# Kernel tuning notes

Measured on AMD Instinct MI355X. Metric: run time of the kernel, lower is better.

## Reference

```python
import jax, jax.numpy as jnp
import numpy as np

EPS = 1e-12  # matches torch F.normalize eps
TEMPERATURE = 1.0


def _l2_normalize(x):
    n = jnp.sqrt(jnp.sum(x * x, axis=-1, keepdims=True))
    return x / jnp.maximum(n, EPS)


def setup_inputs() -> dict:
    key = jax.random.key(0)
    k1, k2 = jax.random.split(key)
    B, L, D, V = 2, 2048, 1024, 32000
    embeddings = jax.random.normal(k1, (B, L, D), dtype=jnp.float32)
    vocab_embeddings = jax.random.normal(k2, (V, D), dtype=jnp.float32)
    return {"embeddings": embeddings, "vocab_embeddings": vocab_embeddings, "k": 8}


def reference(embeddings, vocab_embeddings, k):
    """Soft KNN routing: cosine similarity -> top-k -> temperature softmax
    scattered into a full (B, L, V) probability distribution, plus hard
    argmax token ids (forward())."""
    B, L, D = embeddings.shape
    V = vocab_embeddings.shape[0]
    q = _l2_normalize(embeddings.reshape(-1, D))          # (N, D)
    vocab = _l2_normalize(vocab_embeddings)               # (V, D)
    sims = q @ vocab.T                                    # (N, V) cosine similarities
    topk_sim, topk_idx = jax.lax.top_k(sims, k)           # (N, k)
    probs_k = jax.nn.softmax(topk_sim / TEMPERATURE, axis=-1)
    N = q.shape[0]
    probs = jnp.zeros((N, V), dtype=probs_k.dtype)
    probs = probs.at[jnp.arange(N)[:, None], topk_idx].set(probs_k)
    probs = probs.reshape(B, L, V)                        # forward_soft output
    token_ids = topk_idx[:, 0].reshape(B, L)              # forward() hard routing (k=1)
    return probs, token_ids
```

## Files before the change

kernel.cpp:

```cpp
#include <hip/hip_runtime.h>
#include <math.h>

typedef unsigned short u16;
typedef unsigned int u32;
typedef unsigned char u8;
typedef long i64;
typedef float f32x16 __attribute__((ext_vector_type(16)));

static constexpr int N = 4096;
static constexpr int D = 1024;
static constexpr int V = 32000;
static constexpr int K = 8;
static constexpr int BM = 128;
static constexpr int BV = 256;
static constexpr int BK = 128;
static constexpr int NTILES = V / BV;
static constexpr int NG = 16;
static constexpr int NCAND = NG * K;
static constexpr int T24 = 24;
static constexpr int CPL = NCAND / 64;
static constexpr int GRID = (N / BM) * NG;
static constexpr u32 PSENT = 0x00800000u;

static constexpr size_t OUT_PROB_BYTES = (size_t)N * V * 4;
static constexpr size_t CAND_OFS = 83886080;
static constexpr size_t ZOFS = CAND_OFS + (size_t)N * NCAND * 4;
static constexpr size_t NZ4 = (OUT_PROB_BYTES - ZOFS) / 16;

static_assert(N % BM == 0 && V % BV == 0, "tiling");
static_assert(ZOFS % 16 == 0, "align");
static_assert(NZ4 == (size_t)209 * GRID * 256, "zero quota exact");

__device__ __forceinline__ u8 f2fp8(float f) {
  u32 u = __float_as_uint(f);
  u32 sign = (u >> 24) & 0x80u;
  u32 au = u & 0x7FFFFFFFu;
  if (au < 0x3D800000u) {
    int m = (int)(__uint_as_float(au) * 512.0f + 0.5f);
    return (u8)(sign | (u32)m);
  }
  au += 0x7FFFFu + ((au >> 20) & 1u);
  if (au >= 0x43E00000u) return (u8)(sign | 0x7Eu);
  u32 e = (au >> 23) - 120u;
  return (u8)(sign | (e << 3) | ((au >> 20) & 7u));
}
__device__ __forceinline__ u32 flipbits(float v) {
  u32 u = __float_as_uint(v);
  return u ^ (((u32)((int)u >> 31)) | 0x80000000u);
}
__device__ __forceinline__ float unpackval(u32 p) {
  u32 s = p | 2047u;
  u32 u = (s & 0x80000000u) ? (s ^ 0x80000000u) : ~s;
  return __uint_as_float(u);
}
__device__ __forceinline__ void insert8(u32 pv[K], u32 x) {
  if (x <= pv[K - 1]) return;
  bool g[K];
#pragma unroll
  for (int j = 0; j < K; ++j) g[j] = x > pv[j];
#pragma unroll
  for (int j = K - 1; j >= 1; --j)
    pv[j] = g[j - 1] ? pv[j - 1] : (g[j] ? x : pv[j]);
  if (g[0]) pv[0] = x;
}

__global__ void zero_kernel(float4* __restrict__ p, int n4) {
  int i = blockIdx.x * blockDim.x + threadIdx.x;
  int stride = gridDim.x * blockDim.x;
  float4 z = make_float4(0.f, 0.f, 0.f, 0.f);
  for (; i < n4; i += stride) p[i] = z;
}

__global__ void normcvt_kernel(const float* __restrict__ x, float* __restrict__ inv,
                               u32* __restrict__ o) {
  int row = blockIdx.x;
  const float4* xr = reinterpret_cast<const float4*>(x + (size_t)row * D);
  float4 v = xr[threadIdx.x];
  float ss = v.x * v.x + v.y * v.y + v.z * v.z + v.w * v.w;
#pragma unroll
  for (int off = 32; off > 0; off >>= 1) ss += __shfl_down(ss, off, 64);
  __shared__ float wsum[4];
  if ((threadIdx.x & 63) == 0) wsum[threadIdx.x >> 6] = ss;
  __syncthreads();
  __shared__ float s_inv;
  if (threadIdx.x == 0) {
    float t = wsum[0] + wsum[1] + wsum[2] + wsum[3];
    float iv = 1.0f / fmaxf(sqrtf(t), 1e-12f);
    inv[row] = iv;
    s_inv = iv;
  }
  __syncthreads();
  float s = s_inv * 16.0f;
  u32 b0 = f2fp8(v.x * s), b1 = f2fp8(v.y * s), b2 = f2fp8(v.z * s), b3 = f2fp8(v.w * s);
  o[row * (D / 4) + threadIdx.x] = b0 | (b1 << 8) | (b2 << 16) | (b3 << 24);
}

__global__ __launch_bounds__(256, 2)
void simtopk_kernel(const u8* __restrict__ qn, const u8* __restrict__ vn,
                    u32* __restrict__ cand, float4* __restrict__ zout) {
  __shared__ __align__(16) u8 sh[(BV + BM) * BK];

  u8* v_sh = sh;
  u8* q_sh = sh + BV * BK;

  const int tid = threadIdx.x;
  const int bid = blockIdx.x;
  const int u_ = bid >> 3;
  const int rb = u_ & 31;
  const int grp = (bid & 7) * 2 + (u_ >> 5);
  const int t0 = (grp * NTILES) >> 4;
  const int t1 = ((grp + 1) * NTILES) >> 4;
  const int rbase = rb * BM;
  const int wid = tid >> 6, l = tid & 63;
  const int wv = wid >> 1, wq = wid & 1;
  const int h = l >> 5, lid = l & 31;
  const int srow = l >> 3;
  const int sk = ((l & 7) ^ srow) << 4;

  const float4 zf4 = make_float4(0.f, 0.f, 0.f, 0.f);

  u32 pv[2][K];
#pragma unroll
  for (int n = 0; n < 2; ++n)
#pragma unroll
    for (int j = 0; j < K; ++j) pv[n][j] = PSENT;
  float tminf[2] = {-3.0e38f, -3.0e38f};

  for (int ti = t0; ti < t1; ++ti) {
    const int cb = (ti - t0) * BV;
    f32x16 acc[4][2];
#pragma unroll
    for (int m = 0; m < 4; ++m)
#pragma unroll
      for (int n = 0; n < 2; ++n)
#pragma unroll
        for (int r = 0; r < 16; ++r) acc[m][n][r] = 0.f;

    for (int kk = 0; kk < D / BK; ++kk) {
      __syncthreads();
      {
        int it = (ti - t0) * 8 + kk;
#pragma unroll
        for (int j = 0; j < 4; ++j) {
          int s = it * 4 + j;
          if (s < 209) zout[(size_t)s * (GRID * 256) + bid * 256 + tid] = zf4;
        }
      }
      const int kb = kk * BK;
#pragma unroll
      for (int c = 0; c < 8; ++c) {
        int seg = c * 4 + wid;
        const u8* gs = vn + (size_t)(ti * BV + seg * 8 + srow) * D + kb + sk;
        __builtin_amdgcn_global_load_lds((const __attribute__((address_space(1))) void*)gs,
            (__attribute__((address_space(3))) void*)(v_sh + seg * 1024), 16, 0, 0);
      }
#pragma unroll
      for (int c = 0; c < 4; ++c) {
        int seg = c * 4 + wid;
        const u8* gs = qn + (size_t)(rbase + seg * 8 + srow) * D + kb + sk;
        __builtin_amdgcn_global_load_lds((const __attribute__((address_space(1))) void*)gs,
            (__attribute__((address_space(3))) void*)(q_sh + seg * 1024), 16, 0, 0);
      }
      __syncthreads();
      __builtin_amdgcn_s_setprio(1);
#pragma unroll
      for (int t = 0; t < 8; ++t) {
        i64 vf[4], qf[2];
#pragma unroll
        for (int m = 0; m < 4; ++m) {
          int row = wv * 128 + m * 32 + lid;
          int byte = row * BK + (((t ^ (row & 7)) << 4) | (h << 3));
          vf[m] = *reinterpret_cast<const i64*>(v_sh + byte);
        }
#pragma unroll
        for (int n = 0; n < 2; ++n) {
          int row = wq * 64 + n * 32 + lid;
          int byte = row * BK + (((t ^ (row & 7)) << 4) | (h << 3));
          qf[n] = *reinterpret_cast<const i64*>(q_sh + byte);
        }
#pragma unroll
        for (int m = 0; m < 4; ++m)
#pragma unroll
          for (int n = 0; n < 2; ++n)
            acc[m][n] = __builtin_amdgcn_mfma_f32_32x32x16_fp8_fp8(vf[m], qf[n], acc[m][n], 0, 0, 0);
      }
      __builtin_amdgcn_s_setprio(0);
    }

#pragma unroll
    for (int n = 0; n < 2; ++n) {
#pragma unroll
      for (int m = 0; m < 4; ++m) {
        f32x16 a = acc[m][n];
        float x01 = fmaxf(a[0], a[1]),   x23 = fmaxf(a[2], a[3]);
        float x45 = fmaxf(a[4], a[5]),   x67 = fmaxf(a[6], a[7]);
        float x89 = fmaxf(a[8], a[9]),   xab = fmaxf(a[10], a[11]);
        float xcd = fmaxf(a[12], a[13]), xef = fmaxf(a[14], a[15]);
        float mx = fmaxf(fmaxf(fmaxf(x01, x23), fmaxf(x45, x67)),
                         fmaxf(fmaxf(x89, xab), fmaxf(xcd, xef)));
        if (mx > tminf[n]) {
          const int cidb = cb + wv * 128 + m * 32 + 4 * h;
#pragma unroll
          for (int r = 0; r < 16; ++r) {
            float v = a[r];
            if (v > tminf[n]) {
              int cid = cidb + (r & 3) + 8 * (r >> 2);
              u32 p = (flipbits(v) & 0xFFFFF800u) | (u32)(2047 - cid);
              insert8(pv[n], p);
            }
          }
          tminf[n] = unpackval(pv[n][K - 1]);
        }
      }
    }
  }

  __syncthreads();
  u32* marr = (u32*)sh;
#pragma unroll
  for (int n = 0; n < 2; ++n)
#pragma unroll
    for (int j = 0; j < K; ++j)
      marr[((wq * 64 + n * 32 + lid) * 4 + (wv * 2 + h)) * K + j] = pv[n][j];
  __syncthreads();
  if (tid < BM) {
    u32 fv[K];
#pragma unroll
    for (int j = 0; j < K; ++j) fv[j] = PSENT;
#pragma unroll
    for (int c4 = 0; c4 < 4; ++c4)
#pragma unroll
      for (int j = 0; j < K; ++j) insert8(fv, marr[(tid * 4 + c4) * K + j]);
#pragma unroll
    for (int j = 0; j < K; ++j)
      cand[(size_t)(rbase + tid) * NCAND + grp * K + j] = fv[j];
  }
}

__global__ __launch_bounds__(256)
void rescore_kernel(const u32* __restrict__ cand,
                    const float* __restrict__ emb, const float* __restrict__ vocab,
                    const float* __restrict__ invq, const float* __restrict__ invv,
                    float* __restrict__ res_p, int* __restrict__ res_i) {
  const int tid = threadIdx.x, wid = tid >> 6, l = tid & 63;
  const int row = blockIdx.x * 4 + wid;

  float4 q[4];
#pragma unroll
  for (int t = 0; t < 4; ++t)
    q[t] = *(reinterpret_cast<const float4*>(emb + (size_t)row * D) + t * 64 + l);
  float iqr = invq[row];

  u32 pl[CPL]; int li[CPL];
#pragma unroll
  for (int t = 0; t < CPL; ++t) {
    int e = l * CPL + t;
    u32 p = cand[(size_t)row * NCAND + e];
    int grp = e >> 3;
    int tile0 = (grp * NTILES) >> 4;
    pl[t] = p;
    li[t] = tile0 * BV + 2047 - (int)(p & 2047u);
  }

  int cidx[T24];
#pragma unroll
  for (int jr = 0; jr < T24; ++jr) {
    u32 bp = pl[0]; int bi = li[0];
#pragma unroll
    for (int t = 1; t < CPL; ++t)
      if (pl[t] > bp || (pl[t] == bp && li[t] < bi)) { bp = pl[t]; bi = li[t]; }
#pragma unroll
    for (int off = 32; off > 0; off >>= 1) {
      u32 op = (u32)__shfl_xor((int)bp, off, 64); int oi = __shfl_xor(bi, off, 64);
      if (op > bp || (op == bp && oi < bi)) { bp = op; bi = oi; }
    }
    cidx[jr] = bi;
#pragma unroll
    for (int t = 0; t < CPL; ++t) if (li[t] == bi) pl[t] = 0u;
  }

  float sv[T24];
#pragma unroll
  for (int jr = 0; jr < T24; ++jr) {
    int ix = cidx[jr];
    const float4* vr = reinterpret_cast<const float4*>(vocab + (size_t)ix * D);
    float s = 0.f;
#pragma unroll
    for (int t = 0; t < 4; ++t) {
      float4 vv = vr[t * 64 + l];
      s += q[t].x * vv.x + q[t].y * vv.y + q[t].z * vv.z + q[t].w * vv.w;
    }
#pragma unroll
    for (int off = 32; off > 0; off >>= 1) s += __shfl_xor(s, off, 64);
    sv[jr] = s * iqr * invv[ix];
  }

  float pvv[K]; int pii[K];
#pragma unroll
  for (int r8 = 0; r8 < K; ++r8) {
    float bv = sv[0]; int bi = cidx[0];
#pragma unroll
    for (int jr = 1; jr < T24; ++jr)
      if (sv[jr] > bv || (sv[jr] == bv && cidx[jr] < bi)) { bv = sv[jr]; bi = cidx[jr]; }
    pvv[r8] = bv; pii[r8] = bi;
#pragma unroll
    for (int jr = 0; jr < T24; ++jr) if (cidx[jr] == bi) sv[jr] = -3.0e38f;
  }

  float m = pvv[0], sum = 0.f, e8[K];
#pragma unroll
  for (int j = 0; j < K; ++j) { e8[j] = expf(pvv[j] - m); sum += e8[j]; }
  float isum = 1.f / sum;
  if (l == 0) {
#pragma unroll
    for (int j = 0; j < K; ++j) {
      res_p[row * K + j] = e8[j] * isum;
      res_i[row * K + j] = pii[j];
    }
  }
}

__global__ void scatter_kernel(const float* __restrict__ res_p, const int* __restrict__ res_i,
                               float* __restrict__ out) {
  int row = blockIdx.x * blockDim.x + threadIdx.x;
#pragma unroll
  for (int j = 0; j < K; ++j) out[(size_t)row * V + res_i[row * K + j]] = res_p[row * K + j];
  out[(size_t)N * V + row] = (float)res_i[row * K];
}

extern "C" void kernel_launch(void* const* d_in, const int* in_sizes, int n_in,
                              void* d_out, int out_size, void* d_ws, size_t ws_size,
                              hipStream_t stream) {
  const float* emb   = (const float*)d_in[0];
  const float* vocab = (const float*)d_in[1];
  float* out = (float*)d_out;

  u8* qn = (u8*)d_out;
  u8* vn = qn + (size_t)N * D;
  u32* cand = (u32*)((char*)d_out + CAND_OFS);
  float4* ztail = (float4*)((char*)d_out + ZOFS);

  float* wsf   = (float*)d_ws;
  float* invq  = wsf;
  float* invv  = wsf + N;
  float* res_p = wsf + N + V;
  int*   res_i = (int*)(wsf + N + V + N * K);

  normcvt_kernel<<<N, 256, 0, stream>>>(emb, invq, (u32*)qn);
  normcvt_kernel<<<V, 256, 0, stream>>>(vocab, invv, (u32*)vn);
  simtopk_kernel<<<GRID, 256, 0, stream>>>(qn, vn, cand, ztail);
  rescore_kernel<<<N / 4, 256, 0, stream>>>(cand, emb, vocab, invq, invv, res_p, res_i);
  zero_kernel<<<2048, 256, 0, stream>>>((float4*)d_out, (int)(ZOFS / 16));
  scatter_kernel<<<N / 256, 256, 0, stream>>>(res_p, res_i, out);
}
```

Before: 467.3 us.

## Pre-transpose fp8 operands into MFMA fragment layout and load directly to registers

Measured after the change: 556.9 us. 19.2% more time.

```diff
diff --git a/kernel.cpp b/kernel.cpp
--- a/kernel.cpp
+++ b/kernel.cpp
@@ -1,7 +1,6 @@
 #include <hip/hip_runtime.h>
 #include <math.h>
 
-typedef unsigned short u16;
 typedef unsigned int u32;
 typedef unsigned char u8;
 typedef long i64;
@@ -13,7 +12,6 @@
 static constexpr int K = 8;
 static constexpr int BM = 128;
 static constexpr int BV = 256;
-static constexpr int BK = 128;
 static constexpr int NTILES = V / BV;
 static constexpr int NG = 16;
 static constexpr int NCAND = NG * K;
@@ -71,37 +69,50 @@
   for (; i < n4; i += stride) p[i] = z;
 }
 
-__global__ void normcvt_kernel(const float* __restrict__ x, float* __restrict__ inv,
-                               u32* __restrict__ o) {
-  int row = blockIdx.x;
-  const float4* xr = reinterpret_cast<const float4*>(x + (size_t)row * D);
-  float4 v = xr[threadIdx.x];
-  float ss = v.x * v.x + v.y * v.y + v.z * v.z + v.w * v.w;
-#pragma unroll
-  for (int off = 32; off > 0; off >>= 1) ss += __shfl_down(ss, off, 64);
-  __shared__ float wsum[4];
-  if ((threadIdx.x & 63) == 0) wsum[threadIdx.x >> 6] = ss;
+__global__ __launch_bounds__(256)
+void normcvtT_kernel(const float* __restrict__ x, float* __restrict__ inv,
+                     u8* __restrict__ ot, int rows) {
+  __shared__ u32 lt[32 * 257];
+  const int tid = threadIdx.x, w = tid >> 6, l = tid & 63;
+  const int rb = blockIdx.x * 32;
+  for (int i = 0; i < 8; ++i) {
+    int r = w * 8 + i;
+    const float4* xr = reinterpret_cast<const float4*>(x + (size_t)(rb + r) * D);
+    float4 v[4];
+    float ss = 0.f;
+#pragma unroll
+    for (int j = 0; j < 4; ++j) {
+      v[j] = xr[j * 64 + l];
+      ss += v[j].x * v[j].x + v[j].y * v[j].y + v[j].z * v[j].z + v[j].w * v[j].w;
+    }
+#pragma unroll
+    for (int off = 32; off > 0; off >>= 1) ss += __shfl_xor(ss, off, 64);
+    float iv = 1.0f / fmaxf(sqrtf(ss), 1e-12f);
+    if (l == 0) inv[rb + r] = iv;
+    float sc = iv * 16.0f;
+#pragma unroll
+    for (int j = 0; j < 4; ++j) {
+      u32 p = (u32)f2fp8(v[j].x * sc) | ((u32)f2fp8(v[j].y * sc) << 8) |
+              ((u32)f2fp8(v[j].z * sc) << 16) | ((u32)f2fp8(v[j].w * sc) << 24);
+      lt[r * 257 + j * 64 + l] = p;
+    }
+  }
   __syncthreads();
-  __shared__ float s_inv;
-  if (threadIdx.x == 0) {
-    float t = wsum[0] + wsum[1] + wsum[2] + wsum[3];
-    float iv = 1.0f / fmaxf(sqrtf(t), 1e-12f);
-    inv[row] = iv;
-    s_inv = iv;
-  }
-  __syncthreads();
-  float s = s_inv * 16.0f;
-  u32 b0 = f2fp8(v.x * s), b1 = f2fp8(v.y * s), b2 = f2fp8(v.z * s), b3 = f2fp8(v.w * s);
-  o[row * (D / 4) + threadIdx.x] = b0 | (b1 << 8) | (b2 << 16) | (b3 << 24);
+  const int r = tid & 31, cg = tid >> 5;
+#pragma unroll
+  for (int i = 0; i < 16; ++i) {
+    int c = cg + 8 * i;
+    u32 lo = lt[r * 257 + c * 2];
+    u32 hi = lt[r * 257 + c * 2 + 1];
+    *reinterpret_cast<unsigned long long*>(ot + ((size_t)c * rows + rb + r) * 8) =
+        (unsigned long long)lo | ((unsigned long long)hi << 32);
+  }
 }
 
 __global__ __launch_bounds__(256, 2)
-void simtopk_kernel(const u8* __restrict__ qn, const u8* __restrict__ vn,
+void simtopk_kernel(const u8* __restrict__ qnt, const u8* __restrict__ vnt,
                     u32* __restrict__ cand, float4* __restrict__ zout) {
-  __shared__ __align__(16) u8 sh[(BV + BM) * BK];
-
-  u8* v_sh = sh;
-  u8* q_sh = sh + BV * BK;
+  __shared__ u32 marr[BM * 4 * K];
 
   const int tid = threadIdx.x;
   const int bid = blockIdx.x;
@@ -114,8 +125,6 @@
   const int wid = tid >> 6, l = tid & 63;
   const int wv = wid >> 1, wq = wid & 1;
   const int h = l >> 5, lid = l & 31;
-  const int srow = l >> 3;
-  const int sk = ((l & 7) ^ srow) << 4;
 
   const float4 zf4 = make_float4(0.f, 0.f, 0.f, 0.f);
 
@@ -126,67 +135,35 @@
     for (int j = 0; j < K; ++j) pv[n][j] = PSENT;
   float tminf[2] = {-3.0e38f, -3.0e38f};
 
-  for (int ti = t0; ti < t1; ++ti) {
-    const int cb = (ti - t0) * BV;
-    f32x16 acc[4][2];
+  f32x16 acc[4][2];
+#pragma unroll
+  for (int m = 0; m < 4; ++m)
+#pragma unroll
+    for (int n = 0; n < 2; ++n)
+#pragma unroll
+      for (int r = 0; r < 16; ++r) acc[m][n][r] = 0.f;
+
+  auto LOADF = [&](int ti, int t, i64* vf, i64* qf) {
+    const u8* vp = vnt + ((size_t)(2 * t + h) * V + (size_t)ti * BV + wv * 128 + lid) * 8;
+    const u8* qp = qnt + ((size_t)(2 * t + h) * N + rbase + wq * 64 + lid) * 8;
+#pragma unroll
+    for (int m = 0; m < 4; ++m) vf[m] = *reinterpret_cast<const i64*>(vp + m * 256);
+#pragma unroll
+    for (int n = 0; n < 2; ++n) qf[n] = *reinterpret_cast<const i64*>(qp + n * 256);
+  };
+
+  auto MFMA8 = [&](i64* vf, i64* qf) {
+    __builtin_amdgcn_s_setprio(1);
 #pragma unroll
     for (int m = 0; m < 4; ++m)
 #pragma unroll
       for (int n = 0; n < 2; ++n)
-#pragma unroll
-        for (int r = 0; r < 16; ++r) acc[m][n][r] = 0.f;
-
-    for (int kk = 0; kk < D / BK; ++kk) {
-      __syncthreads();
-      {
-        int it = (ti - t0) * 8 + kk;
-#pragma unroll
-        for (int j = 0; j < 4; ++j) {
-          int s = it * 4 + j;
-          if (s < 209) zout[(size_t)s * (GRID * 256) + bid * 256 + tid] = zf4;
-        }
-      }
-      const int kb = kk * BK;
-#pragma unroll
-      for (int c = 0; c < 8; ++c) {
-        int seg = c * 4 + wid;
-        const u8* gs = vn + (size_t)(ti * BV + seg * 8 + srow) * D + kb + sk;
-        __builtin_amdgcn_global_load_lds((const __attribute__((address_space(1))) void*)gs,
-            (__attribute__((address_space(3))) void*)(v_sh + seg * 1024), 16, 0, 0);
-      }
-#pragma unroll
-      for (int c = 0; c < 4; ++c) {
-        int seg = c * 4 + wid;
-        const u8* gs = qn + (size_t)(rbase + seg * 8 + srow) * D + kb + sk;
-        __builtin_amdgcn_global_load_lds((const __attribute__((address_space(1))) void*)gs,
-            (__attribute__((address_space(3))) void*)(q_sh + seg * 1024), 16, 0, 0);
-      }
-      __syncthreads();
-      __builtin_amdgcn_s_setprio(1);
-#pragma unroll
-      for (int t = 0; t < 8; ++t) {
-        i64 vf[4], qf[2];
-#pragma unroll
-        for (int m = 0; m < 4; ++m) {
-          int row = wv * 128 + m * 32 + lid;
-          int byte = row * BK + (((t ^ (row & 7)) << 4) | (h << 3));
-          vf[m] = *reinterpret_cast<const i64*>(v_sh + byte);
-        }
-#pragma unroll
-        for (int n = 0; n < 2; ++n) {
-          int row = wq * 64 + n * 32 + lid;
-          int byte = row * BK + (((t ^ (row & 7)) << 4) | (h << 3));
-          qf[n] = *reinterpret_cast<const i64*>(q_sh + byte);
-        }
-#pragma unroll
-        for (int m = 0; m < 4; ++m)
-#pragma unroll
-          for (int n = 0; n < 2; ++n)
-            acc[m][n] = __builtin_amdgcn_mfma_f32_32x32x16_fp8_fp8(vf[m], qf[n], acc[m][n], 0, 0, 0);
-      }
-      __builtin_amdgcn_s_setprio(0);
-    }
-
+        acc[m][n] = __builtin_amdgcn_mfma_f32_32x32x16_fp8_fp8(vf[m], qf[n], acc[m][n], 0, 0, 0);
+    __builtin_amdgcn_s_setprio(0);
+  };
+
+  auto SCAN = [&](int tcnt) {
+    const int cb = tcnt * BV;
 #pragma unroll
     for (int n = 0; n < 2; ++n) {
 #pragma unroll
@@ -213,10 +190,32 @@
         }
       }
     }
+#pragma unroll
+    for (int m = 0; m < 4; ++m)
+#pragma unroll
+      for (int n = 0; n < 2; ++n)
+#pragma unroll
+        for (int r = 0; r < 16; ++r) acc[m][n][r] = 0.f;
+  };
+
+  i64 va[4], qa[2], vb[4], qb[2];
+  for (int ti = t0; ti < t1; ++ti) {
+    const int tcnt = ti - t0;
+    LOADF(ti, 0, va, qa);
+    for (int t = 0; t < 64; t += 2) {
+      LOADF(ti, t + 1, vb, qb);
+      {
+        int s = tcnt * 32 + (t >> 1);
+        if (s < 209) zout[(size_t)s * (GRID * 256) + bid * 256 + tid] = zf4;
+      }
+      MFMA8(va, qa);
+      if (t + 2 < 64) LOADF(ti, t + 2, va, qa);
+      MFMA8(vb, qb);
+    }
+    SCAN(tcnt);
   }
 
   __syncthreads();
-  u32* marr = (u32*)sh;
 #pragma unroll
   for (int n = 0; n < 2; ++n)
 #pragma unroll
@@ -335,8 +334,8 @@
   const float* vocab = (const float*)d_in[1];
   float* out = (float*)d_out;
 
-  u8* qn = (u8*)d_out;
-  u8* vn = qn + (size_t)N * D;
+  u8* qnt = (u8*)d_out;
+  u8* vnt = qnt + (size_t)128 * N * 8;
   u32* cand = (u32*)((char*)d_out + CAND_OFS);
   float4* ztail = (float4*)((char*)d_out + ZOFS);
 
@@ -346,9 +345,9 @@
   float* res_p = wsf + N + V;
   int*   res_i = (int*)(wsf + N + V + N * K);
 
-  normcvt_kernel<<<N, 256, 0, stream>>>(emb, invq, (u32*)qn);
-  normcvt_kernel<<<V, 256, 0, stream>>>(vocab, invv, (u32*)vn);
-  simtopk_kernel<<<GRID, 256, 0, stream>>>(qn, vn, cand, ztail);
+  normcvtT_kernel<<<N / 32, 256, 0, stream>>>(emb, invq, qnt, N);
+  normcvtT_kernel<<<V / 32, 256, 0, stream>>>(vocab, invv, vnt, V);
+  simtopk_kernel<<<GRID, 256, 0, stream>>>(qnt, vnt, cand, ztail);
   rescore_kernel<<<N / 4, 256, 0, stream>>>(cand, emb, vocab, invq, invv, res_p, res_i);
   zero_kernel<<<2048, 256, 0, stream>>>((float4*)d_out, (int)(ZOFS / 16));
   scatter_kernel<<<N / 256, 256, 0, stream>>>(res_p, res_i, out);
```
